# Optimization experiments

Measured on AMD Instinct MI355X. Metric: run time of the kernel, lower is better.

Reference implementation:

```python
import jax, jax.numpy as jnp
import numpy as np

B, N, D, H = 1, 1024, 512, 16
DH = D // H
NBINS = 68
R0 = 10.0
K_ITER = 20
LAM = 1.0


def _ln(x, w, b):
    m = x.mean(-1, keepdims=True)
    v = ((x - m) ** 2).mean(-1, keepdims=True)
    return (x - m) * jax.lax.rsqrt(v + 1e-5) * w + b


def _ln_plain(x):
    m = x.mean(-1, keepdims=True)
    v = ((x - m) ** 2).mean(-1, keepdims=True)
    return (x - m) * jax.lax.rsqrt(v + 1e-5)


def setup_inputs():
    key = jax.random.key(0)
    k = jax.random.split(key, 16)
    s = 0.02
    return {
        "h": jax.random.normal(k[0], (B, N, D), jnp.float32),
        "x_res": jax.random.normal(k[1], (B, N, 3), jnp.float32) * 3.0,
        "mu": jax.random.uniform(k[2], (B, H, N), jnp.float32, 0.5, 1.5) / N,
        "nu": jax.random.uniform(k[3], (B, H, N), jnp.float32, 0.5, 1.5) / N,
        "log_u_prev": jnp.zeros((B, H, N), jnp.float32),
        "log_v_prev": jnp.zeros((B, H, N), jnp.float32),
        "mask": jnp.ones((B, N), jnp.float32),
        "ln_attn_w": jnp.ones((D,), jnp.float32),
        "ln_attn_b": jnp.zeros((D,), jnp.float32),
        "wq": jax.random.normal(k[4], (D, D), jnp.float32) * s,
        "wk": jax.random.normal(k[5], (D, D), jnp.float32) * s,
        "wv": jax.random.normal(k[6], (D, D), jnp.float32) * s,
        "wg": jax.random.normal(k[7], (D, D), jnp.float32) * s,
        "wo": jax.random.normal(k[8], (D, D), jnp.float32) * s,
        "gamma": jax.random.normal(k[9], (H,), jnp.float32) * 1e-4,
        "pos_weight": jax.random.normal(k[10], (NBINS, H), jnp.float32) * s,
        "w_dist_logit": jnp.full((H,), -2.0, jnp.float32),
        "ln_ff_w": jnp.ones((D,), jnp.float32),
        "ln_ff_b": jnp.zeros((D,), jnp.float32),
        "sw_w1": jax.random.normal(k[11], (4 * D, D), jnp.float32) * s,
        "sw_w3": jax.random.normal(k[12], (4 * D, D), jnp.float32) * s,
        "sw_w2": jax.random.normal(k[13], (D, 4 * D), jnp.float32) * s,
        "pos_bins": jax.random.randint(k[14], (B, N, N), 0, NBINS, jnp.int32),
        "eps": jnp.array([0.5] * 4 + [1.0] * 4 + [2.0] * 4 + [4.0] * 4, jnp.float32),
    }


def reference(h, x_res, mu, nu, log_u_prev, log_v_prev, mask, ln_attn_w, ln_attn_b,
              wq, wk, wv, wg, wo, gamma, pos_weight, w_dist_logit,
              ln_ff_w, ln_ff_b, sw_w1, sw_w3, sw_w2, pos_bins, eps):
    h_n = _ln(h, ln_attn_w, ln_attn_b)

    def heads(w):
        return (h_n @ w.T).reshape(B, N, H, DH).transpose(0, 2, 1, 3)  # (B,H,N,DH)

    Q = _ln_plain(heads(wq))
    K = _ln_plain(heads(wk))
    V = heads(wv)
    G = heads(wg)

    # similarity + position bias + distance-gated kernel
    S = jnp.einsum('bhid,bhjd->bhij', Q, K) / np.float32(np.sqrt(DH))  # (B,H,N,N)
    bias = pos_weight[pos_bins].transpose(0, 3, 1, 2)                 # (B,H,N,N)
    d2 = jnp.sum((x_res[:, :, None, :] - x_res[:, None, :, :]) ** 2, -1)  # (B,N,N)
    w_dist = jax.nn.sigmoid(w_dist_logit)                             # (H,)
    logits = S + bias - w_dist[None, :, None, None] * d2[:, None, :, :] / (R0 ** 2)

    pair_mask = mask[:, None, :, None] * mask[:, None, None, :]       # (B,1,N,N)
    logK = jnp.where(pair_mask > 0, logits / eps[None, :, None, None], -1e9)

    # unbalanced log-domain Sinkhorn, 20 iterations, warm-started
    fi = (LAM / (LAM + eps))[None, :, None]                           # (1,H,1)
    log_mu = jnp.log(jnp.clip(mu, 1e-8))
    log_nu = jnp.log(jnp.clip(nu, 1e-8))
    log_u, log_v = log_u_prev, log_v_prev
    lse = jax.scipy.special.logsumexp
    for _ in range(K_ITER):
        log_u = fi * (log_mu - lse(logK + log_v[:, :, None, :], axis=-1))
        log_v = fi * (log_nu - lse(logK + log_u[:, :, :, None], axis=-2))

    P = jnp.exp(logK + log_u[:, :, :, None] + log_v[:, :, None, :]) * pair_mask
    row = jnp.clip(P.sum(-1, keepdims=True), 1e-8)
    Pn = P / row                                                      # row-normalized plan

    attn = jnp.einsum('bhij,bhjd->bhid', Pn, V) * jax.nn.sigmoid(G)
    o = attn.transpose(0, 2, 1, 3).reshape(B, N, D)
    h = h + (o @ wo.T) * mask[:, :, None]

    # centroid EGNN coordinate update
    x_cent = jnp.einsum('bhij,bjc->bhic', Pn, x_res)                  # (B,H,N,3)
    delta = x_res[:, None, :, :] - x_cent
    x_upd = jnp.einsum('h,bhnc->bnc', jnp.tanh(gamma) / H, delta) * mask[:, :, None]
    x_res = x_res + x_upd

    # SwiGLU FFN
    h2 = _ln(h, ln_ff_w, ln_ff_b)
    ff = (jax.nn.silu(h2 @ sw_w1.T) * (h2 @ sw_w3.T)) @ sw_w2.T
    h = h + ff * mask[:, :, None]
    return h, x_res, log_u, log_v
```

## Files before the change

kernel.cpp:

```cpp
#include <hip/hip_runtime.h>
#include <cstddef>
#include <cstdint>

#define N_TOK 1024
#define D_MODEL 512
#define H_HEADS 16
#define DHEAD 32
#define DFF 2048

typedef __attribute__((ext_vector_type(8))) short short8;
typedef __attribute__((ext_vector_type(4))) float f32x4_t;

__device__ __forceinline__ float sigmoidf_(float x){ return 1.f/(1.f+__expf(-x)); }

__device__ __forceinline__ unsigned short f2bf(float f){
  union { float f; unsigned u; } v; v.f = f;
  unsigned r = (v.u + 0x7FFFu + ((v.u >> 16) & 1u)) >> 16;
  return (unsigned short)r;
}
__device__ __forceinline__ float bf_lo(unsigned u){ return __uint_as_float(u << 16); }
__device__ __forceinline__ float bf_hi(unsigned u){ return __uint_as_float(u & 0xFFFF0000u); }

__global__ __launch_bounds__(256) void ln_rows(const float* __restrict__ x,
                                               const float* __restrict__ w,
                                               const float* __restrict__ b,
                                               unsigned short* __restrict__ y) {
  int row = blockIdx.x;
  const float* xr = x + (size_t)row * D_MODEL;
  float s = 0.f, s2 = 0.f;
  for (int i = threadIdx.x; i < D_MODEL; i += 256) { float v = xr[i]; s += v; s2 += v*v; }
  #pragma unroll
  for (int off = 32; off; off >>= 1) { s += __shfl_down(s, off); s2 += __shfl_down(s2, off); }
  __shared__ float rs[4], rs2[4];
  int wave = threadIdx.x >> 6, lane = threadIdx.x & 63;
  if (lane == 0) { rs[wave] = s; rs2[wave] = s2; }
  __syncthreads();
  s  = rs[0] + rs[1] + rs[2] + rs[3];
  s2 = rs2[0] + rs2[1] + rs2[2] + rs2[3];
  float mean = s * (1.f / D_MODEL);
  float var  = s2 * (1.f / D_MODEL) - mean * mean;
  float r = rsqrtf(var + 1e-5f);
  unsigned short* yr = y + (size_t)row * D_MODEL;
  for (int i = threadIdx.x; i < D_MODEL; i += 256)
    yr[i] = f2bf((xr[i] - mean) * r * w[i] + b[i]);
}

__global__ __launch_bounds__(256) void conv_weights(const float* __restrict__ wq,
                                                    const float* __restrict__ wk,
                                                    const float* __restrict__ wv,
                                                    const float* __restrict__ wg,
                                                    const float* __restrict__ wo,
                                                    const float* __restrict__ w1,
                                                    const float* __restrict__ w3,
                                                    const float* __restrict__ w2,
                                                    unsigned short* __restrict__ dst) {
  size_t i = ((size_t)blockIdx.x * 256 + threadIdx.x) * 4;
  const float* src; size_t off;
  if      (i < 262144)  { src = wq; off = i; }
  else if (i < 524288)  { src = wk; off = i - 262144; }
  else if (i < 786432)  { src = wv; off = i - 524288; }
  else if (i < 1048576) { src = wg; off = i - 786432; }
  else if (i < 1310720) { src = wo; off = i - 1048576; }
  else if (i < 2359296) { src = w1; off = i - 1310720; }
  else if (i < 3407872) { src = w3; off = i - 2359296; }
  else                  { src = w2; off = i - 3407872; }
  float4 v = *(const float4*)&src[off];
  unsigned lo = ((unsigned)f2bf(v.y) << 16) | f2bf(v.x);
  unsigned hi = ((unsigned)f2bf(v.w) << 16) | f2bf(v.z);
  *(uint2*)&dst[i] = make_uint2(lo, hi);
}

__global__ __launch_bounds__(256) void gemm_mfma(const unsigned short* __restrict__ A,
                                                 const unsigned short* __restrict__ B,
                                                 float* __restrict__ C,
                                                 int M, int K, int Nout,
                                                 const float* __restrict__ addmat,
                                                 const float* __restrict__ maskrow) {
  __shared__ unsigned short As[128][40];
  __shared__ unsigned short Bs[128][40];
  int t = threadIdx.x;
  int m0 = blockIdx.y * 128, n0 = blockIdx.x * 128;
  int wave = t >> 6, lane = t & 63;
  int wm = (wave >> 1) * 64, wn = (wave & 1) * 64;
  int lm = lane & 15, quad = lane >> 4;
  f32x4_t zero = {0.f, 0.f, 0.f, 0.f};
  f32x4_t acc[4][4];
  #pragma unroll
  for (int i = 0; i < 4; ++i)
    #pragma unroll
    for (int j = 0; j < 4; ++j) acc[i][j] = zero;

  int sr = t >> 2, sc = (t & 3) * 8;
  for (int kk = 0; kk < K; kk += 32) {
    #pragma unroll
    for (int c = 0; c < 2; ++c) {
      int r = sr + c * 64;
      *(uint4*)&As[r][sc] = *(const uint4*)&A[(size_t)(m0 + r) * K + kk + sc];
      *(uint4*)&Bs[r][sc] = *(const uint4*)&B[(size_t)(n0 + r) * K + kk + sc];
    }
    __syncthreads();
    short8 af[4], bfr[4];
    #pragma unroll
    for (int mt = 0; mt < 4; ++mt)
      af[mt] = *(const short8*)&As[wm + mt * 16 + lm][quad * 8];
    #pragma unroll
    for (int nt = 0; nt < 4; ++nt)
      bfr[nt] = *(const short8*)&Bs[wn + nt * 16 + lm][quad * 8];
    #pragma unroll
    for (int mt = 0; mt < 4; ++mt)
      #pragma unroll
      for (int nt = 0; nt < 4; ++nt)
        acc[mt][nt] = __builtin_amdgcn_mfma_f32_16x16x32_bf16(af[mt], bfr[nt], acc[mt][nt], 0, 0, 0);
    __syncthreads();
  }
  #pragma unroll
  for (int mt = 0; mt < 4; ++mt) {
    #pragma unroll
    for (int reg = 0; reg < 4; ++reg) {
      int gm = m0 + wm + mt * 16 + quad * 4 + reg;
      float mk = maskrow ? maskrow[gm] : 0.f;
      #pragma unroll
      for (int nt = 0; nt < 4; ++nt) {
        int gn = n0 + wn + nt * 16 + lm;
        float v = acc[mt][nt][reg];
        if (addmat) v = addmat[(size_t)gm * Nout + gn] + v * mk;
        C[(size_t)gm * Nout + gn] = v;
      }
    }
  }
}

__global__ __launch_bounds__(256) void gemm_mfma64(const unsigned short* __restrict__ A,
                                                   const unsigned short* __restrict__ B,
                                                   float* __restrict__ C,
                                                   int M, int K, int Nout,
                                                   const float* __restrict__ addmat,
                                                   const float* __restrict__ maskrow) {
  __shared__ unsigned short As[64][40];
  __shared__ unsigned short Bs[64][40];
  int t = threadIdx.x;
  int m0 = blockIdx.y * 64, n0 = blockIdx.x * 64;
  int wave = t >> 6, lane = t & 63;
  int wm = (wave >> 1) * 32, wn = (wave & 1) * 32;
  int lm = lane & 15, quad = lane >> 4;
  f32x4_t zero = {0.f, 0.f, 0.f, 0.f};
  f32x4_t acc[2][2];
  #pragma unroll
  for (int i = 0; i < 2; ++i)
    #pragma unroll
    for (int j = 0; j < 2; ++j) acc[i][j] = zero;

  int sr = t >> 2, sc = (t & 3) * 8;
  for (int kk = 0; kk < K; kk += 32) {
    *(uint4*)&As[sr][sc] = *(const uint4*)&A[(size_t)(m0 + sr) * K + kk + sc];
    *(uint4*)&Bs[sr][sc] = *(const uint4*)&B[(size_t)(n0 + sr) * K + kk + sc];
    __syncthreads();
    short8 af[2], bfr[2];
    #pragma unroll
    for (int mt = 0; mt < 2; ++mt)
      af[mt] = *(const short8*)&As[wm + mt * 16 + lm][quad * 8];
    #pragma unroll
    for (int nt = 0; nt < 2; ++nt)
      bfr[nt] = *(const short8*)&Bs[wn + nt * 16 + lm][quad * 8];
    #pragma unroll
    for (int mt = 0; mt < 2; ++mt)
      #pragma unroll
      for (int nt = 0; nt < 2; ++nt)
        acc[mt][nt] = __builtin_amdgcn_mfma_f32_16x16x32_bf16(af[mt], bfr[nt], acc[mt][nt], 0, 0, 0);
    __syncthreads();
  }
  #pragma unroll
  for (int mt = 0; mt < 2; ++mt) {
    #pragma unroll
    for (int reg = 0; reg < 4; ++reg) {
      int gm = m0 + wm + mt * 16 + quad * 4 + reg;
      float mk = maskrow ? maskrow[gm] : 0.f;
      #pragma unroll
      for (int nt = 0; nt < 2; ++nt) {
        int gn = n0 + wn + nt * 16 + lm;
        float v = acc[mt][nt][reg];
        if (addmat) v = addmat[(size_t)gm * Nout + gn] + v * mk;
        C[(size_t)gm * Nout + gn] = v;
      }
    }
  }
}

__global__ __launch_bounds__(256) void headln(float* __restrict__ base, int ld) {
  int g = blockIdx.x * 256 + threadIdx.x;
  int i = g & (N_TOK - 1), hh = g >> 10;
  float* p = base + (size_t)i * ld + hh * DHEAD;
  float s = 0.f, s2 = 0.f;
  #pragma unroll
  for (int k = 0; k < DHEAD; ++k) { float v = p[k]; s += v; s2 += v*v; }
  float m = s * (1.f / DHEAD);
  float var = s2 * (1.f / DHEAD) - m * m;
  float r = rsqrtf(var + 1e-5f);
  #pragma unroll
  for (int k = 0; k < DHEAD; ++k) p[k] = (p[k] - m) * r;
}

__global__ __launch_bounds__(256) void build_W_mfma(const float* __restrict__ Q0,
                                                    const float* __restrict__ K0,
                                                    int ld,
                                                    const float* __restrict__ xres,
                                                    const int* __restrict__ bins,
                                                    const float* __restrict__ posw,
                                                    const float* __restrict__ wdl,
                                                    const float* __restrict__ epsp,
                                                    const float* __restrict__ mask,
                                                    unsigned short* __restrict__ Wm,
                                                    unsigned short* __restrict__ WmT) {
  int h = blockIdx.z;
  int i0 = blockIdx.y * 64, j0 = blockIdx.x * 64;
  __shared__ unsigned short Qs[64][40];
  __shared__ unsigned short Ks[64][40];
  __shared__ unsigned char  binsU[64][68];
  __shared__ unsigned short tileB[64][68];
  __shared__ float xi0[64], xi1[64], xi2[64], xj0[64], xj1[64], xj2[64];
  __shared__ float mi_s[64], mj_s[64], poswS[68];
  int t = threadIdx.x;
  {
    int r = t >> 2, c8 = (t & 3) * 8;
    const float* qsrc = Q0 + (size_t)(i0 + r) * ld + h * DHEAD + c8;
    const float* ksrc = K0 + (size_t)(j0 + r) * ld + h * DHEAD + c8;
    float4 qa = *(const float4*)qsrc, qb = *(const float4*)(qsrc + 4);
    float4 ka = *(const float4*)ksrc, kb = *(const float4*)(ksrc + 4);
    unsigned short* qd = &Qs[r][c8];
    qd[0]=f2bf(qa.x); qd[1]=f2bf(qa.y); qd[2]=f2bf(qa.z); qd[3]=f2bf(qa.w);
    qd[4]=f2bf(qb.x); qd[5]=f2bf(qb.y); qd[6]=f2bf(qb.z); qd[7]=f2bf(qb.w);
    unsigned short* kd = &Ks[r][c8];
    kd[0]=f2bf(ka.x); kd[1]=f2bf(ka.y); kd[2]=f2bf(ka.z); kd[3]=f2bf(ka.w);
    kd[4]=f2bf(kb.x); kd[5]=f2bf(kb.y); kd[6]=f2bf(kb.z); kd[7]=f2bf(kb.w);
  }
  {
    int rb = t >> 2, cb = (t & 3) * 16;
    const int* bsrc = bins + (size_t)(i0 + rb) * N_TOK + j0 + cb;
    #pragma unroll
    for (int c = 0; c < 4; ++c) {
      int4 b4 = *(const int4*)(bsrc + c * 4);
      uchar4 u4 = make_uchar4((unsigned char)b4.x, (unsigned char)b4.y,
                              (unsigned char)b4.z, (unsigned char)b4.w);
      *(uchar4*)&binsU[rb][cb + c * 4] = u4;
    }
  }
  if (t < 64) {
    xi0[t] = xres[(i0 + t) * 3 + 0]; xi1[t] = xres[(i0 + t) * 3 + 1]; xi2[t] = xres[(i0 + t) * 3 + 2];
    xj0[t] = xres[(j0 + t) * 3 + 0]; xj1[t] = xres[(j0 + t) * 3 + 1]; xj2[t] = xres[(j0 + t) * 3 + 2];
    mi_s[t] = mask[i0 + t]; mj_s[t] = mask[j0 + t];
  }
  if (t >= 64 && t < 132) poswS[t - 64] = posw[(t - 64) * H_HEADS + h];
  __syncthreads();
  int wave = t >> 6, lane = t & 63;
  int lm = lane & 15, quad = lane >> 4;
  int wm = (wave >> 1) * 32, wn = (wave & 1) * 32;
  f32x4_t zero = {0.f, 0.f, 0.f, 0.f};
  f32x4_t acc[2][2] = {{zero, zero}, {zero, zero}};
  short8 af[2], bfr[2];
  #pragma unroll
  for (int mt = 0; mt < 2; ++mt) af[mt] = *(const short8*)&Qs[wm + mt * 16 + lm][quad * 8];
  #pragma unroll
  for (int nt = 0; nt < 2; ++nt) bfr[nt] = *(const short8*)&Ks[wn + nt * 16 + lm][quad * 8];
  #pragma unroll
  for (int mt = 0; mt < 2; ++mt)
    #pragma unroll
    for (int nt = 0; nt < 2; ++nt)
      acc[mt][nt] = __builtin_amdgcn_mfma_f32_16x16x32_bf16(af[mt], bfr[nt], acc[mt][nt], 0, 0, 0);
  float wd = sigmoidf_(wdl[h]);
  float inv_eps = 1.f / epsp[h];
  const float inv_sqrt = 0.17677669529663687f;
  #pragma unroll
  for (int mt = 0; mt < 2; ++mt) {
    #pragma unroll
    for (int nt = 0; nt < 2; ++nt) {
      int col = wn + nt * 16 + lm;
      float xj0v = xj0[col], xj1v = xj1[col], xj2v = xj2[col], mj = mj_s[col];
      #pragma unroll
      for (int reg = 0; reg < 4; ++reg) {
        int row = wm + mt * 16 + quad * 4 + reg;
        float d0 = xi0[row] - xj0v, d1 = xi1[row] - xj1v, d2c = xi2[row] - xj2v;
        float d2 = d0*d0 + d1*d1 + d2c*d2c;
        float bias = poswS[binsU[row][col]];
        float logit = acc[mt][nt][reg] * inv_sqrt + bias - wd * d2 * 0.01f;
        float outv = (mi_s[row] * mj > 0.f) ? __expf(logit * inv_eps) : 0.f;
        tileB[row][col] = f2bf(outv);
      }
    }
  }
  __syncthreads();
  {
    int r = t >> 2, cb = (t & 3) * 16;
    unsigned short* dst = Wm + ((size_t)h * N_TOK + (i0 + r)) * N_TOK + j0 + cb;
    uint4 w0 = *(uint4*)&tileB[r][cb];
    uint4 w1v = *(uint4*)&tileB[r][cb + 8];
    *(uint4*)dst = w0;
    *(uint4*)(dst + 8) = w1v;
  }
  {
    int jt = t >> 2, cb = (t & 3) * 16;
    unsigned short* dst = WmT + ((size_t)h * N_TOK + (j0 + jt)) * N_TOK + i0 + cb;
    #pragma unroll
    for (int half = 0; half < 2; ++half) {
      int ib = cb + half * 8;
      unsigned a0 = ((unsigned)tileB[ib+1][jt] << 16) | tileB[ib+0][jt];
      unsigned a1 = ((unsigned)tileB[ib+3][jt] << 16) | tileB[ib+2][jt];
      unsigned a2 = ((unsigned)tileB[ib+5][jt] << 16) | tileB[ib+4][jt];
      unsigned a3 = ((unsigned)tileB[ib+7][jt] << 16) | tileB[ib+6][jt];
      *(uint4*)(dst + half * 8) = make_uint4(a0, a1, a2, a3);
    }
  }
}

__global__ __launch_bounds__(256) void build_vxt(const float* __restrict__ QKVG_,
                                                 const float* __restrict__ xres,
                                                 unsigned short* __restrict__ Vxt) {
  int h = blockIdx.x, j0 = blockIdx.y * 64;
  __shared__ float T[48][72];
  int t = threadIdx.x;
  {
    int j = t >> 2, c8 = (t & 3) * 8;
    const float* src = QKVG_ + (size_t)(j0 + j) * 2048 + 1024 + h * DHEAD + c8;
    float4 a = *(const float4*)src, b = *(const float4*)(src + 4);
    T[c8 + 0][j] = a.x; T[c8 + 1][j] = a.y; T[c8 + 2][j] = a.z; T[c8 + 3][j] = a.w;
    T[c8 + 4][j] = b.x; T[c8 + 5][j] = b.y; T[c8 + 6][j] = b.z; T[c8 + 7][j] = b.w;
  }
  if (t < 64) {
    int j = t;
    T[32][j] = xres[(j0 + j) * 3 + 0];
    T[33][j] = xres[(j0 + j) * 3 + 1];
    T[34][j] = xres[(j0 + j) * 3 + 2];
    T[35][j] = 1.f;
    #pragma unroll
    for (int d = 36; d < 48; ++d) T[d][j] = 0.f;
  }
  __syncthreads();
  for (int task = t; task < 384; task += 256) {
    int d = task >> 3, jc = (task & 7) * 8;
    float* s = &T[d][jc];
    unsigned a0 = ((unsigned)f2bf(s[1]) << 16) | f2bf(s[0]);
    unsigned a1 = ((unsigned)f2bf(s[3]) << 16) | f2bf(s[2]);
    unsigned a2 = ((unsigned)f2bf(s[5]) << 16) | f2bf(s[4]);
    unsigned a3 = ((unsigned)f2bf(s[7]) << 16) | f2bf(s[6]);
    *(uint4*)(Vxt + ((size_t)h * 48 + d) * N_TOK + j0 + jc) = make_uint4(a0, a1, a2, a3);
  }
}

__global__ __launch_bounds__(256) void sink_init(const float* __restrict__ mu,
                                                 const float* __restrict__ nu,
                                                 const float* __restrict__ lv0,
                                                 float* __restrict__ lmu,
                                                 float* __restrict__ lnu,
                                                 float* __restrict__ vtilde) {
  int i = blockIdx.x * 256 + threadIdx.x;
  lmu[i] = __logf(fmaxf(mu[i], 1e-8f));
  lnu[i] = __logf(fmaxf(nu[i], 1e-8f));
  vtilde[i] = __expf(lv0[i]);
}

__global__ __launch_bounds__(256) void sink_lin(const unsigned short* __restrict__ Wsrc,
                                                const float* __restrict__ othert,
                                                const float* __restrict__ lmarg,
                                                float* __restrict__ outlog,
                                                float* __restrict__ outexp,
                                                const float* __restrict__ epsp) {
  int t = threadIdx.x;
  int rblk = blockIdx.x * 16;
  int h = rblk >> 10;
  int wave = t >> 6, lane = t & 63;
  int sub = lane >> 4, l16 = lane & 15;
  int row = rblk + wave * 4 + sub;
  int i = row & (N_TOK - 1);
  const uint4* p = (const uint4*)(Wsrc + (size_t)row * N_TOK);
  const float4* vt = (const float4*)(othert + h * N_TOK);
  float s8[8];
  #pragma unroll
  for (int c = 0; c < 8; ++c) s8[c] = 0.f;
  #pragma unroll
  for (int it = 0; it < 8; ++it) {
    int j0 = it * 128 + l16 * 8;
    uint4 u = p[j0 >> 3];
    float4 va = vt[j0 >> 2];
    float4 vb = vt[(j0 >> 2) + 1];
    s8[0] += bf_lo(u.x) * va.x; s8[1] += bf_hi(u.x) * va.y;
    s8[2] += bf_lo(u.y) * va.z; s8[3] += bf_hi(u.y) * va.w;
    s8[4] += bf_lo(u.z) * vb.x; s8[5] += bf_hi(u.z) * vb.y;
    s8[6] += bf_lo(u.w) * vb.z; s8[7] += bf_hi(u.w) * vb.w;
  }
  float s = ((s8[0] + s8[1]) + (s8[2] + s8[3])) + ((s8[4] + s8[5]) + (s8[6] + s8[7]));
  #pragma unroll
  for (int off = 1; off <= 8; off <<= 1) s += __shfl_xor(s, off);
  if (l16 == 0) {
    float fi = 1.f / (1.f + epsp[h]);
    float val = fi * (lmarg[h * N_TOK + i] - __logf(fmaxf(s, 1e-35f)));
    outlog[h * N_TOK + i] = val;
    outexp[h * N_TOK + i] = __expf(val);
  }
}

__global__ __launch_bounds__(256) void finalize_mfma(const unsigned short* __restrict__ Wm,
                                                     const float* __restrict__ vtilde,
                                                     const unsigned short* __restrict__ Vxt,
                                                     const float* __restrict__ G0, int ld,
                                                     const float* __restrict__ xres,
                                                     const float* __restrict__ mask,
                                                     unsigned short* __restrict__ o,
                                                     float* __restrict__ x_out,
                                                     const float* __restrict__ gamma) {
  int mt = blockIdx.x;
  int h = blockIdx.y;
  int t = threadIdx.x, wave = t >> 6, lane = t & 63;
  int lm = lane & 15, quad = lane >> 4;
  __shared__ float vts[N_TOK];
  ((float4*)vts)[t] = ((const float4*)(vtilde + h * N_TOK))[t];
  __syncthreads();
  int arow = mt * 64 + wave * 16 + lm;
  const unsigned short* Kr = Wm + ((size_t)h * N_TOK + arow) * N_TOK + quad * 8;
  const unsigned short* Bb = Vxt + (size_t)h * 48 * N_TOK + quad * 8;
  f32x4_t zero = {0.f, 0.f, 0.f, 0.f};
  f32x4_t acc[3] = {zero, zero, zero};
  for (int kk = 0; kk < N_TOK; kk += 32) {
    uint4 u = *(const uint4*)(Kr + kk);
    float4 la = *(const float4*)&vts[kk + quad * 8];
    float4 lb = *(const float4*)&vts[kk + quad * 8 + 4];
    float p0 = bf_lo(u.x) * la.x;
    float p1 = bf_hi(u.x) * la.y;
    float p2 = bf_lo(u.y) * la.z;
    float p3 = bf_hi(u.y) * la.w;
    float p4 = bf_lo(u.z) * lb.x;
    float p5 = bf_hi(u.z) * lb.y;
    float p6 = bf_lo(u.w) * lb.z;
    float p7 = bf_hi(u.w) * lb.w;
    union { uint4 u4; short8 s8; } pk;
    pk.u4 = make_uint4(((unsigned)f2bf(p1) << 16) | f2bf(p0),
                       ((unsigned)f2bf(p3) << 16) | f2bf(p2),
                       ((unsigned)f2bf(p5) << 16) | f2bf(p4),
                       ((unsigned)f2bf(p7) << 16) | f2bf(p6));
    short8 af = pk.s8;
    #pragma unroll
    for (int nt = 0; nt < 3; ++nt) {
      short8 bfrag = *(const short8*)(Bb + (size_t)(nt * 16 + lm) * N_TOK + kk);
      acc[nt] = __builtin_amdgcn_mfma_f32_16x16x32_bf16(af, bfrag, acc[nt], 0, 0, 0);
    }
  }
  float inv[4];
  #pragma unroll
  for (int reg = 0; reg < 4; ++reg) {
    float rsum = __shfl(acc[2][reg], (quad << 4) | 3, 64);
    inv[reg] = 1.f / fmaxf(rsum, 1e-30f);
  }
  #pragma unroll
  for (int nt = 0; nt < 2; ++nt) {
    int c = nt * 16 + lm;
    #pragma unroll
    for (int reg = 0; reg < 4; ++reg) {
      int r = mt * 64 + wave * 16 + quad * 4 + reg;
      float gv = G0[(size_t)r * ld + h * DHEAD + c];
      float ovl = acc[nt][reg] * inv[reg] * sigmoidf_(gv);
      o[(size_t)r * D_MODEL + h * DHEAD + c] = f2bf(ovl);
    }
  }
  if (lm < 3) {
    float tg = tanhf(gamma[h]) * (1.f / H_HEADS);
    #pragma unroll
    for (int reg = 0; reg < 4; ++reg) {
      int r = mt * 64 + wave * 16 + quad * 4 + reg;
      float xc = acc[2][reg] * inv[reg];
      float mi = mask[r];
      atomicAdd(&x_out[r * 3 + lm], tg * mi * (xres[r * 3 + lm] - xc));
    }
  }
}

__global__ __launch_bounds__(256) void silu_mul_bf(const float* __restrict__ ffab,
                                                   unsigned short* __restrict__ out, int n) {
  int i = blockIdx.x * 256 + threadIdx.x;
  if (i >= n) return;
  int row = i >> 11, col = i & 2047;
  float a = ffab[(size_t)row * 4096 + col];
  float bb = ffab[(size_t)row * 4096 + 2048 + col];
  out[i] = f2bf(a * sigmoidf_(a) * bb);
}

__global__ __launch_bounds__(256) void copyf(const float* __restrict__ src,
                                             float* __restrict__ dst, int n) {
  int i = blockIdx.x * 256 + threadIdx.x;
  if (i < n) dst[i] = src[i];
}

extern "C" void kernel_launch(void* const* d_in, const int* in_sizes, int n_in,
                              void* d_out, int out_size, void* d_ws, size_t ws_size,
                              hipStream_t stream) {
  const float* h_in  = (const float*)d_in[0];
  const float* x_res = (const float*)d_in[1];
  const float* mu    = (const float*)d_in[2];
  const float* nu    = (const float*)d_in[3];
  const float* lu0   = (const float*)d_in[4];
  const float* lv0   = (const float*)d_in[5];
  const float* mask  = (const float*)d_in[6];
  const float* lnw   = (const float*)d_in[7];
  const float* lnb   = (const float*)d_in[8];
  const float* wq    = (const float*)d_in[9];
  const float* wk    = (const float*)d_in[10];
  const float* wv    = (const float*)d_in[11];
  const float* wg    = (const float*)d_in[12];
  const float* wo    = (const float*)d_in[13];
  const float* gamma = (const float*)d_in[14];
  const float* posw  = (const float*)d_in[15];
  const float* wdl   = (const float*)d_in[16];
  const float* lnfw  = (const float*)d_in[17];
  const float* lnfb  = (const float*)d_in[18];
  const float* w1    = (const float*)d_in[19];
  const float* w3    = (const float*)d_in[20];
  const float* w2    = (const float*)d_in[21];
  const int*   bins  = (const int*)d_in[22];
  const float* eps   = (const float*)d_in[23];

  float* out    = (float*)d_out;
  float* out_h  = out;
  float* out_x  = out + 524288;
  float* out_lu = out + 527360;
  float* out_lv = out + 543744;

  float* ws = (float*)d_ws;
  float* QKVG  = ws;
  float* h_mid = ws + 2097152;
  unsigned short* U = (unsigned short*)(ws + 2621440);
  unsigned short* h_n_b  = U;
  unsigned short* h2_b   = U + 524288;
  unsigned short* o_b    = U + 1048576;
  unsigned short* wB     = U + 1572864;
  unsigned short* Wb   = (unsigned short*)(ws + 5636096);
  unsigned short* WTb  = Wb + (size_t)H_HEADS * N_TOK * N_TOK;
  unsigned short* Vxt  = WTb + (size_t)H_HEADS * N_TOK * N_TOK;
  float* vtilde = (float*)(Vxt + 786432);
  float* utilde = vtilde + 16384;
  float* lmu    = utilde + 16384;
  float* lnu    = lmu + 16384;
  float* ffab          = (float*)Wb;
  unsigned short* ff_b = WTb;

  unsigned short* wQKVGb = wB;
  unsigned short* wob    = wB + 1048576;
  unsigned short* wFFb   = wB + 1310720;
  unsigned short* w2b    = wB + 3407872;

  dim3 b256(256);

  conv_weights<<<4352, b256, 0, stream>>>(wq, wk, wv, wg, wo, w1, w3, w2, wB);
  ln_rows<<<N_TOK, b256, 0, stream>>>(h_in, lnw, lnb, h_n_b);

  gemm_mfma<<<dim3(16, 8), b256, 0, stream>>>(h_n_b, wQKVGb, QKVG,
                                              N_TOK, D_MODEL, 2048, nullptr, nullptr);

  headln<<<128, b256, 0, stream>>>(QKVG, 2048);

  copyf<<<12, b256, 0, stream>>>(x_res, out_x, N_TOK * 3);

  build_W_mfma<<<dim3(16, 16, H_HEADS), b256, 0, stream>>>(
      QKVG, QKVG + 512, 2048, x_res, bins, posw, wdl, eps, mask, Wb, WTb);
  build_vxt<<<dim3(H_HEADS, N_TOK / 64), b256, 0, stream>>>(QKVG, x_res, Vxt);

  sink_init<<<64, b256, 0, stream>>>(mu, nu, lv0, lmu, lnu, vtilde);
  for (int it = 0; it < 20; ++it) {
    sink_lin<<<1024, b256, 0, stream>>>(Wb, vtilde, lmu, out_lu, utilde, eps);
    sink_lin<<<1024, b256, 0, stream>>>(WTb, utilde, lnu, out_lv, vtilde, eps);
  }

  finalize_mfma<<<dim3(16, H_HEADS), b256, 0, stream>>>(
      Wb, vtilde, Vxt, QKVG + 1536, 2048, x_res, mask, o_b, out_x, gamma);

  gemm_mfma64<<<dim3(8, 16), b256, 0, stream>>>(o_b, wob, h_mid,
                                                N_TOK, D_MODEL, D_MODEL, h_in, mask);

  ln_rows<<<N_TOK, b256, 0, stream>>>(h_mid, lnfw, lnfb, h2_b);

  gemm_mfma<<<dim3(32, 8), b256, 0, stream>>>(h2_b, wFFb, ffab,
                                              N_TOK, D_MODEL, 4096, nullptr, nullptr);
  silu_mul_bf<<<(N_TOK * DFF) / 256, b256, 0, stream>>>(ffab, ff_b, N_TOK * DFF);

  gemm_mfma64<<<dim3(8, 16), b256, 0, stream>>>(ff_b, w2b, out_h,
                                                N_TOK, DFF, D_MODEL, h_mid, mask);
}
```

Measured before the change: 526.5 us.

## Drop transposed kernel matrix; compute column sums from W with head-swizzled blocks

Removes the transposed copy of the per-head Gibbs kernel matrix and replaces the column Sinkhorn step with a new column-reduction kernel that reads the row-major matrix directly. Each block covers 64 columns and reduces partial sums across 16 row groups in shared memory. Block indices are remapped so that blocks are interleaved across heads (a head swizzle), which appears aimed at keeping each head's 2 MB matrix resident in cache across the row and column passes. This halves the workspace written by build_W and the memory streamed per iteration. The trade-off is that the column kernel does strided 8-byte row reads and launches only 256 blocks.

```diff
diff --git a/kernel.cpp b/kernel.cpp
--- a/kernel.cpp
+++ b/kernel.cpp
@@ -20,6 +20,8 @@
 }
 __device__ __forceinline__ float bf_lo(unsigned u){ return __uint_as_float(u << 16); }
 __device__ __forceinline__ float bf_hi(unsigned u){ return __uint_as_float(u & 0xFFFF0000u); }
+
+__device__ __forceinline__ int swz_head(int b){ return (b & 7) + 8 * ((b >> 3) & 1); }
 
 __global__ __launch_bounds__(256) void ln_rows(const float* __restrict__ x,
                                                const float* __restrict__ w,
@@ -209,10 +211,11 @@
                                                     const float* __restrict__ wdl,
                                                     const float* __restrict__ epsp,
                                                     const float* __restrict__ mask,
-                                                    unsigned short* __restrict__ Wm,
-                                                    unsigned short* __restrict__ WmT) {
-  int h = blockIdx.z;
-  int i0 = blockIdx.y * 64, j0 = blockIdx.x * 64;
+                                                    unsigned short* __restrict__ Wm) {
+  int b = blockIdx.x;
+  int h = swz_head(b);
+  int tile = b >> 4;
+  int i0 = (tile >> 4) * 64, j0 = (tile & 15) * 64;
   __shared__ unsigned short Qs[64][40];
   __shared__ unsigned short Ks[64][40];
   __shared__ unsigned char  binsU[64][68];
@@ -296,19 +299,6 @@
     *(uint4*)dst = w0;
     *(uint4*)(dst + 8) = w1v;
   }
-  {
-    int jt = t >> 2, cb = (t & 3) * 16;
-    unsigned short* dst = WmT + ((size_t)h * N_TOK + (j0 + jt)) * N_TOK + i0 + cb;
-    #pragma unroll
-    for (int half = 0; half < 2; ++half) {
-      int ib = cb + half * 8;
-      unsigned a0 = ((unsigned)tileB[ib+1][jt] << 16) | tileB[ib+0][jt];
-      unsigned a1 = ((unsigned)tileB[ib+3][jt] << 16) | tileB[ib+2][jt];
-      unsigned a2 = ((unsigned)tileB[ib+5][jt] << 16) | tileB[ib+4][jt];
-      unsigned a3 = ((unsigned)tileB[ib+7][jt] << 16) | tileB[ib+6][jt];
-      *(uint4*)(dst + half * 8) = make_uint4(a0, a1, a2, a3);
-    }
-  }
 }
 
 __global__ __launch_bounds__(256) void build_vxt(const float* __restrict__ QKVG_,
@@ -357,21 +347,21 @@
   vtilde[i] = __expf(lv0[i]);
 }
 
-__global__ __launch_bounds__(256) void sink_lin(const unsigned short* __restrict__ Wsrc,
-                                                const float* __restrict__ othert,
-                                                const float* __restrict__ lmarg,
+__global__ __launch_bounds__(256) void sink_row(const unsigned short* __restrict__ Wm,
+                                                const float* __restrict__ vtilde,
+                                                const float* __restrict__ lmu,
                                                 float* __restrict__ outlog,
                                                 float* __restrict__ outexp,
                                                 const float* __restrict__ epsp) {
+  int b = blockIdx.x;
+  int h = swz_head(b);
+  int grp = b >> 4;
   int t = threadIdx.x;
-  int rblk = blockIdx.x * 16;
-  int h = rblk >> 10;
   int wave = t >> 6, lane = t & 63;
   int sub = lane >> 4, l16 = lane & 15;
-  int row = rblk + wave * 4 + sub;
-  int i = row & (N_TOK - 1);
-  const uint4* p = (const uint4*)(Wsrc + (size_t)row * N_TOK);
-  const float4* vt = (const float4*)(othert + h * N_TOK);
+  int i = grp * 16 + wave * 4 + sub;
+  const uint4* p = (const uint4*)(Wm + ((size_t)h * N_TOK + i) * N_TOK);
+  const float4* vt = (const float4*)(vtilde + h * N_TOK);
   float s8[8];
   #pragma unroll
   for (int c = 0; c < 8; ++c) s8[c] = 0.f;
@@ -391,9 +381,47 @@
   for (int off = 1; off <= 8; off <<= 1) s += __shfl_xor(s, off);
   if (l16 == 0) {
     float fi = 1.f / (1.f + epsp[h]);
-    float val = fi * (lmarg[h * N_TOK + i] - __logf(fmaxf(s, 1e-35f)));
+    float val = fi * (lmu[h * N_TOK + i] - __logf(fmaxf(s, 1e-35f)));
     outlog[h * N_TOK + i] = val;
     outexp[h * N_TOK + i] = __expf(val);
+  }
+}
+
+__global__ __launch_bounds__(256) void sink_col(const unsigned short* __restrict__ Wm,
+                                                const float* __restrict__ utilde,
+                                                const float* __restrict__ lnu,
+                                                float* __restrict__ outlog,
+                                                float* __restrict__ outexp,
+                                                const float* __restrict__ epsp) {
+  int b = blockIdx.x;
+  int h = swz_head(b);
+  int j0 = (b >> 4) * 64;
+  int t = threadIdx.x;
+  int jl = (t & 15) * 4;
+  int ig = t >> 4;
+  const unsigned short* base = Wm + ((size_t)h * N_TOK + ig * 64) * N_TOK + j0 + jl;
+  const float* ut = utilde + h * N_TOK + ig * 64;
+  float a0 = 0.f, a1 = 0.f, a2 = 0.f, a3 = 0.f;
+  #pragma unroll 8
+  for (int r = 0; r < 64; ++r) {
+    uint2 w = *(const uint2*)(base + (size_t)r * N_TOK);
+    float u = ut[r];
+    a0 += bf_lo(w.x) * u; a1 += bf_hi(w.x) * u;
+    a2 += bf_lo(w.y) * u; a3 += bf_hi(w.y) * u;
+  }
+  __shared__ float red[16][68];
+  red[ig][jl + 0] = a0; red[ig][jl + 1] = a1;
+  red[ig][jl + 2] = a2; red[ig][jl + 3] = a3;
+  __syncthreads();
+  if (t < 64) {
+    float s = 0.f;
+    #pragma unroll
+    for (int g = 0; g < 16; ++g) s += red[g][t];
+    int j = j0 + t;
+    float fi = 1.f / (1.f + epsp[h]);
+    float val = fi * (lnu[h * N_TOK + j] - __logf(fmaxf(s, 1e-35f)));
+    outlog[h * N_TOK + j] = val;
+    outexp[h * N_TOK + j] = __expf(val);
   }
 }
 
@@ -406,8 +434,9 @@
                                                      unsigned short* __restrict__ o,
                                                      float* __restrict__ x_out,
                                                      const float* __restrict__ gamma) {
-  int mt = blockIdx.x;
-  int h = blockIdx.y;
+  int b = blockIdx.x;
+  int h = swz_head(b);
+  int mt = b >> 4;
   int t = threadIdx.x, wave = t >> 6, lane = t & 63;
   int lm = lane & 15, quad = lane >> 4;
   __shared__ float vts[N_TOK];
@@ -530,14 +559,13 @@
   unsigned short* o_b    = U + 1048576;
   unsigned short* wB     = U + 1572864;
   unsigned short* Wb   = (unsigned short*)(ws + 5636096);
-  unsigned short* WTb  = Wb + (size_t)H_HEADS * N_TOK * N_TOK;
-  unsigned short* Vxt  = WTb + (size_t)H_HEADS * N_TOK * N_TOK;
+  unsigned short* Vxt  = Wb + (size_t)H_HEADS * N_TOK * N_TOK;
   float* vtilde = (float*)(Vxt + 786432);
   float* utilde = vtilde + 16384;
   float* lmu    = utilde + 16384;
   float* lnu    = lmu + 16384;
+  unsigned short* ff_b = (unsigned short*)(lnu + 16384);
   float* ffab          = (float*)Wb;
-  unsigned short* ff_b = WTb;
 
   unsigned short* wQKVGb = wB;
   unsigned short* wob    = wB + 1048576;
@@ -556,17 +584,17 @@
 
   copyf<<<12, b256, 0, stream>>>(x_res, out_x, N_TOK * 3);
 
-  build_W_mfma<<<dim3(16, 16, H_HEADS), b256, 0, stream>>>(
-      QKVG, QKVG + 512, 2048, x_res, bins, posw, wdl, eps, mask, Wb, WTb);
+  build_W_mfma<<<4096, b256, 0, stream>>>(
+      QKVG, QKVG + 512, 2048, x_res, bins, posw, wdl, eps, mask, Wb);
   build_vxt<<<dim3(H_HEADS, N_TOK / 64), b256, 0, stream>>>(QKVG, x_res, Vxt);
 
   sink_init<<<64, b256, 0, stream>>>(mu, nu, lv0, lmu, lnu, vtilde);
   for (int it = 0; it < 20; ++it) {
-    sink_lin<<<1024, b256, 0, stream>>>(Wb, vtilde, lmu, out_lu, utilde, eps);
-    sink_lin<<<1024, b256, 0, stream>>>(WTb, utilde, lnu, out_lv, vtilde, eps);
-  }
-
-  finalize_mfma<<<dim3(16, H_HEADS), b256, 0, stream>>>(
+    sink_row<<<1024, b256, 0, stream>>>(Wb, vtilde, lmu, out_lu, utilde, eps);
+    sink_col<<<256, b256, 0, stream>>>(Wb, utilde, lnu, out_lv, vtilde, eps);
+  }
+
+  finalize_mfma<<<256, b256, 0, stream>>>(
       Wb, vtilde, Vxt, QKVG + 1536, 2048, x_res, mask, o_b, out_x, gamma);
 
   gemm_mfma64<<<dim3(8, 16), b256, 0, stream>>>(o_b, wob, h_mid,
```

Result: faster. 449.3 us (-14.7%).
